# Performance work log

Measured on AMD Instinct MI355X. Metric: run time of the kernel, lower is better.

Reference implementation:

```python
import jax, jax.numpy as jnp
import numpy as np

B, S, H = 2, 1024, 2048
NH, NKV, HD = 16, 8, 128
GROUPS = NH // NKV
THETA = 1000000.0
SPARSITY = 0.4  # q_len > 512 -> vision_sparse_attention_sparsity_ratio
TOP_K = max(1, min(S, int(SPARSITY * S)))


def _rope(q, k, position_ids):
    # inv_freq: [HD/2]
    inv_freq = 1.0 / (THETA ** (jnp.arange(0, HD, 2, dtype=jnp.float32) / HD))
    freqs = position_ids.astype(jnp.float32)[:, :, None] * inv_freq  # [B,S,HD/2]
    emb = jnp.concatenate([freqs, freqs], axis=-1)                   # [B,S,HD]
    cos = jnp.cos(emb)[:, None].astype(q.dtype)  # [B,1,S,HD] (unsqueeze_dim=1)
    sin = jnp.sin(emb)[:, None].astype(q.dtype)
    rot = lambda x: jnp.concatenate([-x[..., HD // 2:], x[..., :HD // 2]], axis=-1)
    return q * cos + rot(q) * sin, k * cos + rot(k) * sin


def setup_inputs() -> dict:
    key = jax.random.key(0)
    ks = jax.random.split(key, 10)
    sc = 0.02
    inp = {
        'hidden_states': jax.random.normal(ks[0], (B, S, H), jnp.float32),
        'wq': jax.random.normal(ks[1], (NH * HD, H), jnp.float32) * sc,
        'bq': jax.random.normal(ks[2], (NH * HD,), jnp.float32) * sc,
        'wk': jax.random.normal(ks[3], (NKV * HD, H), jnp.float32) * sc,
        'bk': jax.random.normal(ks[4], (NKV * HD,), jnp.float32) * sc,
        'wv': jax.random.normal(ks[5], (NKV * HD, H), jnp.float32) * sc,
        'bv': jax.random.normal(ks[6], (NKV * HD,), jnp.float32) * sc,
        'wo': jax.random.normal(ks[7], (H, NH * HD), jnp.float32) * sc,
        'bo': jax.random.normal(ks[8], (H,), jnp.float32) * sc,
        'position_ids': jnp.tile(jnp.arange(S, dtype=jnp.int32)[None, :], (B, 1)),
    }
    return inp


def reference(hidden_states, wq, bq, wk, bk, wv, bv, wo, bo, position_ids):
    # QKV projections -> [B, heads, S, HD]
    q = (hidden_states @ wq.T + bq).reshape(B, S, NH, HD).transpose(0, 2, 1, 3)
    k = (hidden_states @ wk.T + bk).reshape(B, S, NKV, HD).transpose(0, 2, 1, 3)
    v = (hidden_states @ wv.T + bv).reshape(B, S, NKV, HD).transpose(0, 2, 1, 3)

    q, k = _rope(q, k, position_ids)

    # GQA: repeat_interleave KV heads along head axis
    k = jnp.repeat(k, GROUPS, axis=1)
    v = jnp.repeat(v, GROUPS, axis=1)

    scores = jnp.einsum('bhqd,bhkd->bhqk', q, k) / jnp.sqrt(jnp.float32(HD))

    # VectorizedSparseAttention: keep top-k weights per query, -inf elsewhere
    topk_vals = jax.lax.top_k(scores, TOP_K)[0]          # sorted descending
    thresh = topk_vals[..., -1:]                         # k-th largest per row
    sparse = jnp.where(scores >= thresh, scores, -jnp.inf)

    probs = jax.nn.softmax(sparse.astype(jnp.float32), axis=-1).astype(q.dtype)
    attn = jnp.einsum('bhqk,bhkd->bhqd', probs, v)       # [B,NH,S,HD]
    attn = attn.transpose(0, 2, 1, 3).reshape(B, S, NH * HD)
    return attn @ wo.T + bo
```

## Files before the change

### kernel.cpp

```cpp
#include <hip/hip_runtime.h>
#include <hip/hip_bf16.h>

constexpr int B_ = 2, S_ = 1024, H_ = 2048;
constexpr int NH_ = 16, NKV_ = 8, HD_ = 128, GROUPS_ = 2;
constexpr int TOPK_ = 409;
constexpr int QSTRIDE = NH_ * HD_;
constexpr int KSTRIDE = NKV_ * HD_;
constexpr int QB_ = 16;

typedef __attribute__((ext_vector_type(8))) short short8;
typedef __attribute__((ext_vector_type(4))) float f32x4;
typedef __attribute__((ext_vector_type(4))) unsigned u32x4;
typedef __attribute__((ext_vector_type(4))) unsigned short ush4;

__device__ inline unsigned fkey(float x) {
  unsigned u = __float_as_uint(x);
  return (u & 0x80000000u) ? ~u : (u | 0x80000000u);
}
__device__ inline unsigned short bf16_rne(float x) {
  unsigned u = __float_as_uint(x);
  unsigned r = u + 0x7FFFu + ((u >> 16) & 1u);
  return (unsigned short)(r >> 16);
}
__device__ inline float bf16_to_f(unsigned short h) {
  return __uint_as_float((unsigned)h << 16);
}
__device__ inline unsigned packsplit(float x) {
  unsigned u = __float_as_uint(x);
  unsigned r = (u + 0x7FFFu + ((u >> 16) & 1u)) & 0xFFFF0000u;
  float rem = x - __uint_as_float(r);
  unsigned v = __float_as_uint(rem);
  unsigned l = (v + 0x7FFFu + ((v >> 16) & 1u)) >> 16;
  return r | l;
}

#define PERM_HI 0x07060302u
#define PERM_LO 0x05040100u

__device__ inline void unpack8(const unsigned* p, short8& hi, short8& lo) {
  u32x4 w0 = *(const u32x4*)p;
  u32x4 w1 = *(const u32x4*)(p + 4);
  u32x4 h, l;
  h.x = __builtin_amdgcn_perm(w0.y, w0.x, PERM_HI);
  h.y = __builtin_amdgcn_perm(w0.w, w0.z, PERM_HI);
  h.z = __builtin_amdgcn_perm(w1.y, w1.x, PERM_HI);
  h.w = __builtin_amdgcn_perm(w1.w, w1.z, PERM_HI);
  l.x = __builtin_amdgcn_perm(w0.y, w0.x, PERM_LO);
  l.y = __builtin_amdgcn_perm(w0.w, w0.z, PERM_LO);
  l.z = __builtin_amdgcn_perm(w1.y, w1.x, PERM_LO);
  l.w = __builtin_amdgcn_perm(w1.w, w1.z, PERM_LO);
  hi = *(short8*)&h;
  lo = *(short8*)&l;
}
__device__ inline void unpack8r(u32x4 w0, u32x4 w1, short8& hi, short8& lo) {
  u32x4 h, l;
  h.x = __builtin_amdgcn_perm(w0.y, w0.x, PERM_HI);
  h.y = __builtin_amdgcn_perm(w0.w, w0.z, PERM_HI);
  h.z = __builtin_amdgcn_perm(w1.y, w1.x, PERM_HI);
  h.w = __builtin_amdgcn_perm(w1.w, w1.z, PERM_HI);
  l.x = __builtin_amdgcn_perm(w0.y, w0.x, PERM_LO);
  l.y = __builtin_amdgcn_perm(w0.w, w0.z, PERM_LO);
  l.z = __builtin_amdgcn_perm(w1.y, w1.x, PERM_LO);
  l.w = __builtin_amdgcn_perm(w1.w, w1.z, PERM_LO);
  hi = *(short8*)&h;
  lo = *(short8*)&l;
}

template <int TI>
__device__ __forceinline__ void gemm_split_body(
    const float* __restrict__ A, const float* __restrict__ W,
    const float* __restrict__ bias, float* __restrict__ C, int ldc, int c0,
    int K, int m0) {
  __shared__ unsigned short Ah[2][TI * 32 * 32];
  __shared__ unsigned short Al[2][TI * 32 * 32];
  __shared__ unsigned short Wh[2][128 * 32];
  __shared__ unsigned short Wl[2][128 * 32];
  const int tid = threadIdx.x;
  const int lane = tid & 63, wid = tid >> 6;
  const int wrow = (wid >> 1) * (TI * 16), wcol = (wid & 1) * 64;
  const int fm = lane & 15, quad = lane >> 4;
  const int srow = tid >> 3;
  const int skq = (tid & 7) * 4;
  f32x4 acc[TI][4] = {};
  float4 avr[TI], wvr[4];

  auto loadAW = [&](int k0) {
#pragma unroll
    for (int r = 0; r < TI; ++r)
      avr[r] = *(const float4*)&A[(size_t)(m0 + srow + 32 * r) * K + k0 + skq];
#pragma unroll
    for (int r = 0; r < 4; ++r)
      wvr[r] = *(const float4*)&W[(size_t)(srow + 32 * r) * K + k0 + skq];
  };
  auto convWrite = [&](int buf) {
#pragma unroll
    for (int r = 0; r < TI; ++r) {
      const int row = srow + 32 * r;
      const int off =
          row * 32 + ((((skq >> 3) ^ ((row >> 1) & 3)) << 3) | (skq & 7));
      unsigned short h0 = bf16_rne(avr[r].x), h1 = bf16_rne(avr[r].y),
                     h2 = bf16_rne(avr[r].z), h3 = bf16_rne(avr[r].w);
      ush4 hv; hv.x = h0; hv.y = h1; hv.z = h2; hv.w = h3;
      ush4 lv;
      lv.x = bf16_rne(avr[r].x - bf16_to_f(h0));
      lv.y = bf16_rne(avr[r].y - bf16_to_f(h1));
      lv.z = bf16_rne(avr[r].z - bf16_to_f(h2));
      lv.w = bf16_rne(avr[r].w - bf16_to_f(h3));
      *(ush4*)&Ah[buf][off] = hv;
      *(ush4*)&Al[buf][off] = lv;
    }
#pragma unroll
    for (int r = 0; r < 4; ++r) {
      const int row = srow + 32 * r;
      const int off =
          row * 32 + ((((skq >> 3) ^ ((row >> 1) & 3)) << 3) | (skq & 7));
      unsigned short g0 = bf16_rne(wvr[r].x), g1 = bf16_rne(wvr[r].y),
                     g2 = bf16_rne(wvr[r].z), g3 = bf16_rne(wvr[r].w);
      ush4 hv; hv.x = g0; hv.y = g1; hv.z = g2; hv.w = g3;
      ush4 lv;
      lv.x = bf16_rne(wvr[r].x - bf16_to_f(g0));
      lv.y = bf16_rne(wvr[r].y - bf16_to_f(g1));
      lv.z = bf16_rne(wvr[r].z - bf16_to_f(g2));
      lv.w = bf16_rne(wvr[r].w - bf16_to_f(g3));
      *(ush4*)&Wh[buf][off] = hv;
      *(ush4*)&Wl[buf][off] = lv;
    }
  };

  loadAW(0);
  convWrite(0);
  __syncthreads();
  int cur = 0;
  for (int k0 = 0; k0 < K; k0 += 32) {
    const bool more = (k0 + 32) < K;
    if (more) loadAW(k0 + 32);
    short8 ah[TI], al[TI], bh[4], bl[4];
#pragma unroll
    for (int ti = 0; ti < TI; ++ti) {
      const int r = wrow + 16 * ti + fm;
      const int off = r * 32 + ((quad ^ ((r >> 1) & 3)) << 3);
      ah[ti] = *(const short8*)&Ah[cur][off];
      al[ti] = *(const short8*)&Al[cur][off];
    }
#pragma unroll
    for (int tj = 0; tj < 4; ++tj) {
      const int r = wcol + 16 * tj + fm;
      const int off = r * 32 + ((quad ^ ((r >> 1) & 3)) << 3);
      bh[tj] = *(const short8*)&Wh[cur][off];
      bl[tj] = *(const short8*)&Wl[cur][off];
    }
#pragma unroll
    for (int ti = 0; ti < TI; ++ti)
#pragma unroll
      for (int tj = 0; tj < 4; ++tj) {
        acc[ti][tj] = __builtin_amdgcn_mfma_f32_16x16x32_bf16(
            ah[ti], bh[tj], acc[ti][tj], 0, 0, 0);
        acc[ti][tj] = __builtin_amdgcn_mfma_f32_16x16x32_bf16(
            ah[ti], bl[tj], acc[ti][tj], 0, 0, 0);
        acc[ti][tj] = __builtin_amdgcn_mfma_f32_16x16x32_bf16(
            al[ti], bh[tj], acc[ti][tj], 0, 0, 0);
      }
    if (more) convWrite(cur ^ 1);
    __syncthreads();
    cur ^= 1;
  }
#pragma unroll
  for (int tj = 0; tj < 4; ++tj) {
    float bsv = bias[wcol + 16 * tj + fm];
#pragma unroll
    for (int ti = 0; ti < TI; ++ti) {
      int mrow = m0 + wrow + 16 * ti + quad * 4;
      int ncol = c0 + wcol + 16 * tj + fm;
#pragma unroll
      for (int reg = 0; reg < 4; ++reg)
        C[(size_t)(mrow + reg) * ldc + ncol] = acc[ti][tj][reg] + bsv;
    }
  }
}

__global__ __launch_bounds__(256) void gemm_qkv(
    const float* __restrict__ hidden, const float* __restrict__ wq,
    const float* __restrict__ bq, const float* __restrict__ wk,
    const float* __restrict__ bk, const float* __restrict__ wv,
    const float* __restrict__ bv, float* __restrict__ q, float* __restrict__ k,
    float* __restrict__ v) {
  const int n0 = blockIdx.x * 128, m0 = blockIdx.y * 128;
  const float* W;
  const float* bias;
  float* C;
  int ldc, c0;
  if (n0 < QSTRIDE) {
    W = wq + (size_t)n0 * H_; bias = bq + n0; C = q; ldc = QSTRIDE; c0 = n0;
  } else if (n0 < QSTRIDE + KSTRIDE) {
    int nn = n0 - QSTRIDE;
    W = wk + (size_t)nn * H_; bias = bk + nn; C = k; ldc = KSTRIDE; c0 = nn;
  } else {
    int nn = n0 - QSTRIDE - KSTRIDE;
    W = wv + (size_t)nn * H_; bias = bv + nn; C = v; ldc = KSTRIDE; c0 = nn;
  }
  gemm_split_body<4>(hidden, W, bias, C, ldc, c0, H_, m0);
}

template <int TI>
__global__ __launch_bounds__(256) void gemm_split_k(
    const float* __restrict__ A, const float* __restrict__ W,
    const float* __restrict__ bias, float* __restrict__ C, int N, int K) {
  const int n0 = blockIdx.x * 128, m0 = blockIdx.y * (TI * 32);
  gemm_split_body<TI>(A, W + (size_t)n0 * K, bias + n0, C, N, n0, K, m0);
}

__global__ __launch_bounds__(256) void rope_pack(float* __restrict__ qtmp,
                                                 float* __restrict__ ktmp,
                                                 const int* __restrict__ pos_ids) {
  const int s = blockIdx.x, b = blockIdx.y;
  const int t = threadIdx.x;
  __shared__ float fsh[64];
  if (t < 64) fsh[t] = (float)(1.0 / pow(1.0e6, (double)t / 64.0));
  __syncthreads();
  const int pos = pos_ids[b * S_ + s];
#pragma unroll
  for (int it = 0; it < 6; ++it) {
    const int p = t + 256 * it;
    const int slot = p >> 6;
    const int d = p & 63;
    float* base = (slot < NH_)
                      ? qtmp + (size_t)(b * S_ + s) * QSTRIDE + slot * HD_
                      : ktmp + (size_t)(b * S_ + s) * KSTRIDE + (slot - NH_) * HD_;
    float x = base[d], y = base[d + 64];
    unsigned* up = (unsigned*)base;
    float ang = (float)pos * fsh[d];
    float c = cosf(ang), sn = sinf(ang);
    up[d] = packsplit(x * c - y * sn);
    up[d + 64] = packsplit(y * c + x * sn);
  }
}

__global__ __launch_bounds__(256) void vtrans(const float* __restrict__ vtmp,
                                              unsigned* __restrict__ vT) {
  const int s0 = blockIdx.x * 64;
  const int g = blockIdx.y, b = blockIdx.z;
  __shared__ unsigned tile[64][133];
  const int t = threadIdx.x;
  {
    const int row = t >> 5;
    const int c4 = (t & 31) * 4;
    for (int r = 0; r < 64; r += 8) {
      const float* src =
          vtmp + ((size_t)(b * S_ + s0 + row + r) * NKV_ + g) * HD_ + c4;
      float4 xv = *(const float4*)src;
      tile[row + r][c4 + 0] = packsplit(xv.x);
      tile[row + r][c4 + 1] = packsplit(xv.y);
      tile[row + r][c4 + 2] = packsplit(xv.z);
      tile[row + r][c4 + 3] = packsplit(xv.w);
    }
  }
  __syncthreads();
  {
    const int tok4 = (t & 15) * 4;
    const int d0 = t >> 4;
    for (int dd = 0; dd < 128; dd += 16) {
      const int dim = d0 + dd;
      u32x4 o;
      o.x = tile[tok4 + 0][dim];
      o.y = tile[tok4 + 1][dim];
      o.z = tile[tok4 + 2][dim];
      o.w = tile[tok4 + 3][dim];
      *(u32x4*)&vT[(((size_t)(b * NKV_ + g) * HD_ + dim) * S_) + s0 + tok4] = o;
    }
  }
}

constexpr int SCW = 1030;

__global__ __launch_bounds__(512, 4) void attn_kernel(
    unsigned* __restrict__ qpk, const unsigned* __restrict__ kpk,
    const unsigned* __restrict__ vTpk) {
  const int q0 = blockIdx.x * QB_;
  const int h = blockIdx.y, b = blockIdx.z, g = h / GROUPS_;
  const int t = threadIdx.x, lane = t & 63, wid = t >> 6;
  const int fm = lane & 15, quad = lane >> 4;

  __shared__ float sc[QB_ * SCW];
  __shared__ float redmx[8][QB_];
  __shared__ float Zsh[QB_];
  const float scale = 0.08838834764831845f;

  short8 qh[4], ql[4];
  {
    const unsigned* qrow =
        qpk + (size_t)(b * S_ + q0 + fm) * QSTRIDE + h * HD_;
#pragma unroll
    for (int ks = 0; ks < 4; ++ks) {
      u32x4 a0 = *(const u32x4*)&qrow[ks * 32 + quad * 8];
      u32x4 a1 = *(const u32x4*)&qrow[ks * 32 + quad * 8 + 4];
      unpack8r(a0, a1, qh[ks], ql[ks]);
    }
  }

  const unsigned* kg = kpk + (size_t)(b * S_) * KSTRIDE + g * HD_;
  const int krow = wid * 16 + fm;
  const unsigned* kr0 = kg + (size_t)krow * KSTRIDE;
  u32x4 ka[8], kb[8];
#pragma unroll
  for (int ks = 0; ks < 4; ++ks) {
    ka[2 * ks] = *(const u32x4*)&kr0[ks * 32 + quad * 8];
    ka[2 * ks + 1] = *(const u32x4*)&kr0[ks * 32 + quad * 8 + 4];
  }
  f32x4 mxacc = {-1e30f, -1e30f, -1e30f, -1e30f};
#pragma unroll
  for (int tile = 0; tile < 8; ++tile) {
    u32x4* cur = (tile & 1) ? kb : ka;
    u32x4* nxt = (tile & 1) ? ka : kb;
    if (tile < 7) {
      const unsigned* krn = kr0 + (size_t)(tile + 1) * 128 * KSTRIDE;
#pragma unroll
      for (int ks = 0; ks < 4; ++ks) {
        nxt[2 * ks] = *(const u32x4*)&krn[ks * 32 + quad * 8];
        nxt[2 * ks + 1] = *(const u32x4*)&krn[ks * 32 + quad * 8 + 4];
      }
    }
    f32x4 acc = {0.f, 0.f, 0.f, 0.f};
#pragma unroll
    for (int ks = 0; ks < 4; ++ks) {
      short8 bh, bl;
      unpack8r(cur[2 * ks], cur[2 * ks + 1], bh, bl);
      acc = __builtin_amdgcn_mfma_f32_16x16x32_bf16(qh[ks], bh, acc, 0, 0, 0);
      acc = __builtin_amdgcn_mfma_f32_16x16x32_bf16(qh[ks], bl, acc, 0, 0, 0);
      acc = __builtin_amdgcn_mfma_f32_16x16x32_bf16(ql[ks], bh, acc, 0, 0, 0);
    }
    const int key = tile * 128 + krow;
#pragma unroll
    for (int reg = 0; reg < 4; ++reg) {
      float sval = acc[reg] * scale;
      sc[(quad * 4 + reg) * SCW + key] = sval;
      mxacc[reg] = fmaxf(mxacc[reg], sval);
    }
  }
#pragma unroll
  for (int o = 1; o < 16; o <<= 1) {
    mxacc[0] = fmaxf(mxacc[0], __shfl_xor(mxacc[0], o));
    mxacc[1] = fmaxf(mxacc[1], __shfl_xor(mxacc[1], o));
    mxacc[2] = fmaxf(mxacc[2], __shfl_xor(mxacc[2], o));
    mxacc[3] = fmaxf(mxacc[3], __shfl_xor(mxacc[3], o));
  }
  if (fm == 0) {
#pragma unroll
    for (int reg = 0; reg < 4; ++reg) redmx[wid][quad * 4 + reg] = mxacc[reg];
  }
  __syncthreads();

  const int dim = wid * 16 + fm;
  const unsigned* vTr = vTpk + ((size_t)(b * NKV_ + g) * HD_ + dim) * S_;
  u32x4 va[8], vb[8];
#pragma unroll
  for (int ks = 0; ks < 4; ++ks) {
    va[2 * ks] = *(const u32x4*)&vTr[ks * 32 + quad * 8];
    va[2 * ks + 1] = *(const u32x4*)&vTr[ks * 32 + quad * 8 + 4];
  }

  unsigned curA = 0u, curB = 0u;
  {
    unsigned uvA[16], uvB[16];
#pragma unroll
    for (int j = 0; j < 16; ++j)
      uvA[j] = fkey(sc[(2 * wid) * SCW + lane + 64 * j]);
#pragma unroll
    for (int j = 0; j < 16; ++j)
      uvB[j] = fkey(sc[(2 * wid + 1) * SCW + lane + 64 * j]);
    for (int bit = 31; bit >= 0; --bit) {
      const unsigned cA = curA | (1u << bit), cB = curB | (1u << bit);
      int cntA = 0, cntB = 0;
#pragma unroll
      for (int j = 0; j < 16; ++j)
        cntA += __popcll(__ballot(uvA[j] >= cA));
#pragma unroll
      for (int j = 0; j < 16; ++j)
        cntB += __popcll(__ballot(uvB[j] >= cB));
      if (cntA >= TOPK_) curA = cA;
      if (cntB >= TOPK_) curB = cB;
    }
  }
  const unsigned pref = (lane >= 32) ? curB : curA;

  {
    const int qi = t >> 5, li = t & 31;
    const float mx =
        fmaxf(fmaxf(fmaxf(redmx[0][qi], redmx[1][qi]),
                    fmaxf(redmx[2][qi], redmx[3][qi])),
              fmaxf(fmaxf(redmx[4][qi], redmx[5][qi]),
                    fmaxf(redmx[6][qi], redmx[7][qi])));
    unsigned* scp = (unsigned*)&sc[qi * SCW];
    float zloc = 0.f;
#pragma unroll 2
    for (int j = 0; j < 8; ++j) {
      int i4 = li * 4 + 128 * j;
      f32x4 sv = *(const f32x4*)&sc[qi * SCW + i4];
      u32x4 pk;
      float p0 = (fkey(sv.x) >= pref) ? __expf(sv.x - mx) : 0.0f;
      float p1 = (fkey(sv.y) >= pref) ? __expf(sv.y - mx) : 0.0f;
      float p2 = (fkey(sv.z) >= pref) ? __expf(sv.z - mx) : 0.0f;
      float p3 = (fkey(sv.w) >= pref) ? __expf(sv.w - mx) : 0.0f;
      zloc += p0 + p1 + p2 + p3;
      pk.x = packsplit(p0); pk.y = packsplit(p1);
      pk.z = packsplit(p2); pk.w = packsplit(p3);
      *(u32x4*)&scp[i4] = pk;
    }
#pragma unroll
    for (int off = 1; off < 32; off <<= 1) zloc += __shfl_xor(zloc, off);
    if (li == 0) Zsh[qi] = zloc;
  }
  __syncthreads();

  const unsigned* scp2 = (const unsigned*)sc;
  f32x4 oacc = {0.f, 0.f, 0.f, 0.f};
#pragma unroll
  for (int tile = 0; tile < 8; ++tile) {
    u32x4* cur = (tile & 1) ? vb : va;
    u32x4* nxt = (tile & 1) ? va : vb;
    if (tile < 7) {
      const unsigned* vn = vTr + (tile + 1) * 128;
#pragma unroll
      for (int ks = 0; ks < 4; ++ks) {
        nxt[2 * ks] = *(const u32x4*)&vn[ks * 32 + quad * 8];
        nxt[2 * ks + 1] = *(const u32x4*)&vn[ks * 32 + quad * 8 + 4];
      }
    }
#pragma unroll
    for (int ks = 0; ks < 4; ++ks) {
      short8 ph, pl;
      unpack8(&scp2[fm * SCW + tile * 128 + ks * 32 + quad * 8], ph, pl);
      short8 vh, vl;
      unpack8r(cur[2 * ks], cur[2 * ks + 1], vh, vl);
      oacc = __builtin_amdgcn_mfma_f32_16x16x32_bf16(ph, vh, oacc, 0, 0, 0);
      oacc = __builtin_amdgcn_mfma_f32_16x16x32_bf16(ph, vl, oacc, 0, 0, 0);
      oacc = __builtin_amdgcn_mfma_f32_16x16x32_bf16(pl, vh, oacc, 0, 0, 0);
    }
  }

#pragma unroll
  for (int reg = 0; reg < 4; ++reg) {
    const int q = quad * 4 + reg;
    const float invZ = 1.0f / Zsh[q];
    float* outp = (float*)qpk + (size_t)(b * S_ + q0 + q) * QSTRIDE + h * HD_;
    outp[dim] = oacc[reg] * invZ;
  }
}

extern "C" void kernel_launch(void* const* d_in, const int* in_sizes, int n_in,
                              void* d_out, int out_size, void* d_ws,
                              size_t ws_size, hipStream_t stream) {
  const float* hidden = (const float*)d_in[0];
  const float* wq = (const float*)d_in[1];
  const float* bq = (const float*)d_in[2];
  const float* wk = (const float*)d_in[3];
  const float* bk = (const float*)d_in[4];
  const float* wv = (const float*)d_in[5];
  const float* bv = (const float*)d_in[6];
  const float* wo = (const float*)d_in[7];
  const float* bo = (const float*)d_in[8];
  const int* pos = (const int*)d_in[9];
  float* out = (float*)d_out;

  char* ws = (char*)d_ws;
  float* qtmp = (float*)ws;
  float* ktmp = (float*)(ws + ((size_t)16 << 20));
  float* vtmp = (float*)(ws + ((size_t)24 << 20));
  unsigned* vT = (unsigned*)(ws + ((size_t)32 << 20));

  dim3 blk(256);
  gemm_qkv<<<dim3(32, 16), blk, 0, stream>>>(hidden, wq, bq, wk, bk, wv, bv,
                                             qtmp, ktmp, vtmp);
  rope_pack<<<dim3(S_, B_), dim3(256), 0, stream>>>(qtmp, ktmp, pos);
  vtrans<<<dim3(S_ / 64, NKV_, B_), dim3(256), 0, stream>>>(vtmp, vT);
  attn_kernel<<<dim3(S_ / QB_, NH_, B_), dim3(512), 0, stream>>>(
      (unsigned*)qtmp, (const unsigned*)ktmp, vT);
  gemm_split_k<2><<<dim3(H_ / 128, (B_ * S_) / 64), blk, 0, stream>>>(
      qtmp, wo, bo, out, H_, H_);
}
```

Measured before the change: 569.7 us.

## Pre-pack GEMM operands to split bf16, restructure attention loops and top-k count

Adds a pack_inputs kernel that converts hidden states and all weights to packed hi/lo bf16 pairs once per call, so the GEMM inner loops only permute bytes instead of doing float-to-bf16 splitting. The attention kernel writes its output already packed, so the output projection reads packed data. The QK and PV loops are restructured into non-unrolled ping-pong pairs to shrink code size and register pressure. The top-k radix count moves from per-element ballots to per-lane counts reduced with shuffles. The trade-off is an extra full pass over the weights before the GEMMs, plus workspace buffer reuse: vT shares memory with wqP, which is safe only because gemm_qkv finishes before vtrans runs.

```diff
diff --git a/kernel.cpp b/kernel.cpp
--- a/kernel.cpp
+++ b/kernel.cpp
@@ -11,19 +11,11 @@
 typedef __attribute__((ext_vector_type(8))) short short8;
 typedef __attribute__((ext_vector_type(4))) float f32x4;
 typedef __attribute__((ext_vector_type(4))) unsigned u32x4;
-typedef __attribute__((ext_vector_type(4))) unsigned short ush4;
+typedef __attribute__((ext_vector_type(2))) unsigned u32x2;
 
 __device__ inline unsigned fkey(float x) {
   unsigned u = __float_as_uint(x);
   return (u & 0x80000000u) ? ~u : (u | 0x80000000u);
-}
-__device__ inline unsigned short bf16_rne(float x) {
-  unsigned u = __float_as_uint(x);
-  unsigned r = u + 0x7FFFu + ((u >> 16) & 1u);
-  return (unsigned short)(r >> 16);
-}
-__device__ inline float bf16_to_f(unsigned short h) {
-  return __uint_as_float((unsigned)h << 16);
 }
 __device__ inline unsigned packsplit(float x) {
   unsigned u = __float_as_uint(x);
@@ -66,9 +58,33 @@
   lo = *(short8*)&l;
 }
 
+__global__ __launch_bounds__(256) void pack_inputs(
+    const float* __restrict__ hidden, const float* __restrict__ wq,
+    const float* __restrict__ wk, const float* __restrict__ wv,
+    const float* __restrict__ wo, unsigned* __restrict__ hidP,
+    unsigned* __restrict__ wqP, unsigned* __restrict__ wkP,
+    unsigned* __restrict__ wvP, unsigned* __restrict__ woP) {
+  size_t gid = (size_t)blockIdx.x * 256 + threadIdx.x;
+  const float* src;
+  unsigned* dst;
+  size_t off;
+  if (gid < 1048576) { src = hidden; dst = hidP; off = gid; }
+  else if (gid < 2097152) { src = wq; dst = wqP; off = gid - 1048576; }
+  else if (gid < 2621440) { src = wk; dst = wkP; off = gid - 2097152; }
+  else if (gid < 3145728) { src = wv; dst = wvP; off = gid - 2621440; }
+  else { src = wo; dst = woP; off = gid - 3145728; }
+  float4 x = *(const float4*)&src[off * 4];
+  u32x4 p;
+  p.x = packsplit(x.x);
+  p.y = packsplit(x.y);
+  p.z = packsplit(x.z);
+  p.w = packsplit(x.w);
+  *(u32x4*)&dst[off * 4] = p;
+}
+
 template <int TI>
 __device__ __forceinline__ void gemm_split_body(
-    const float* __restrict__ A, const float* __restrict__ W,
+    const unsigned* __restrict__ A, const unsigned* __restrict__ W,
     const float* __restrict__ bias, float* __restrict__ C, int ldc, int c0,
     int K, int m0) {
   __shared__ unsigned short Ah[2][TI * 32 * 32];
@@ -82,15 +98,15 @@
   const int srow = tid >> 3;
   const int skq = (tid & 7) * 4;
   f32x4 acc[TI][4] = {};
-  float4 avr[TI], wvr[4];
+  u32x4 avr[TI], wvr[4];
 
   auto loadAW = [&](int k0) {
 #pragma unroll
     for (int r = 0; r < TI; ++r)
-      avr[r] = *(const float4*)&A[(size_t)(m0 + srow + 32 * r) * K + k0 + skq];
+      avr[r] = *(const u32x4*)&A[(size_t)(m0 + srow + 32 * r) * K + k0 + skq];
 #pragma unroll
     for (int r = 0; r < 4; ++r)
-      wvr[r] = *(const float4*)&W[(size_t)(srow + 32 * r) * K + k0 + skq];
+      wvr[r] = *(const u32x4*)&W[(size_t)(srow + 32 * r) * K + k0 + skq];
   };
   auto convWrite = [&](int buf) {
 #pragma unroll
@@ -98,32 +114,28 @@
       const int row = srow + 32 * r;
       const int off =
           row * 32 + ((((skq >> 3) ^ ((row >> 1) & 3)) << 3) | (skq & 7));
-      unsigned short h0 = bf16_rne(avr[r].x), h1 = bf16_rne(avr[r].y),
-                     h2 = bf16_rne(avr[r].z), h3 = bf16_rne(avr[r].w);
-      ush4 hv; hv.x = h0; hv.y = h1; hv.z = h2; hv.w = h3;
-      ush4 lv;
-      lv.x = bf16_rne(avr[r].x - bf16_to_f(h0));
-      lv.y = bf16_rne(avr[r].y - bf16_to_f(h1));
-      lv.z = bf16_rne(avr[r].z - bf16_to_f(h2));
-      lv.w = bf16_rne(avr[r].w - bf16_to_f(h3));
-      *(ush4*)&Ah[buf][off] = hv;
-      *(ush4*)&Al[buf][off] = lv;
+      u32x4 w = avr[r];
+      u32x2 hi, lo;
+      hi.x = __builtin_amdgcn_perm(w.y, w.x, PERM_HI);
+      hi.y = __builtin_amdgcn_perm(w.w, w.z, PERM_HI);
+      lo.x = __builtin_amdgcn_perm(w.y, w.x, PERM_LO);
+      lo.y = __builtin_amdgcn_perm(w.w, w.z, PERM_LO);
+      *(u32x2*)&Ah[buf][off] = hi;
+      *(u32x2*)&Al[buf][off] = lo;
     }
 #pragma unroll
     for (int r = 0; r < 4; ++r) {
       const int row = srow + 32 * r;
       const int off =
           row * 32 + ((((skq >> 3) ^ ((row >> 1) & 3)) << 3) | (skq & 7));
-      unsigned short g0 = bf16_rne(wvr[r].x), g1 = bf16_rne(wvr[r].y),
-                     g2 = bf16_rne(wvr[r].z), g3 = bf16_rne(wvr[r].w);
-      ush4 hv; hv.x = g0; hv.y = g1; hv.z = g2; hv.w = g3;
-      ush4 lv;
-      lv.x = bf16_rne(wvr[r].x - bf16_to_f(g0));
-      lv.y = bf16_rne(wvr[r].y - bf16_to_f(g1));
-      lv.z = bf16_rne(wvr[r].z - bf16_to_f(g2));
-      lv.w = bf16_rne(wvr[r].w - bf16_to_f(g3));
-      *(ush4*)&Wh[buf][off] = hv;
-      *(ush4*)&Wl[buf][off] = lv;
+      u32x4 w = wvr[r];
+      u32x2 hi, lo;
+      hi.x = __builtin_amdgcn_perm(w.y, w.x, PERM_HI);
+      hi.y = __builtin_amdgcn_perm(w.w, w.z, PERM_HI);
+      lo.x = __builtin_amdgcn_perm(w.y, w.x, PERM_LO);
+      lo.y = __builtin_amdgcn_perm(w.w, w.z, PERM_LO);
+      *(u32x2*)&Wh[buf][off] = hi;
+      *(u32x2*)&Wl[buf][off] = lo;
     }
   };
 
@@ -179,31 +191,29 @@
 }
 
 __global__ __launch_bounds__(256) void gemm_qkv(
-    const float* __restrict__ hidden, const float* __restrict__ wq,
-    const float* __restrict__ bq, const float* __restrict__ wk,
-    const float* __restrict__ bk, const float* __restrict__ wv,
+    const unsigned* __restrict__ hidP, const unsigned* __restrict__ wqP,
+    const float* __restrict__ bq, const unsigned* __restrict__ wkP,
+    const float* __restrict__ bk, const unsigned* __restrict__ wvP,
     const float* __restrict__ bv, float* __restrict__ q, float* __restrict__ k,
     float* __restrict__ v) {
   const int n0 = blockIdx.x * 128, m0 = blockIdx.y * 128;
-  const float* W;
-  const float* bias;
-  float* C;
-  int ldc, c0;
   if (n0 < QSTRIDE) {
-    W = wq + (size_t)n0 * H_; bias = bq + n0; C = q; ldc = QSTRIDE; c0 = n0;
+    gemm_split_body<4>(hidP, wqP + (size_t)n0 * H_, bq + n0, q, QSTRIDE, n0,
+                       H_, m0);
   } else if (n0 < QSTRIDE + KSTRIDE) {
     int nn = n0 - QSTRIDE;
-    W = wk + (size_t)nn * H_; bias = bk + nn; C = k; ldc = KSTRIDE; c0 = nn;
+    gemm_split_body<4>(hidP, wkP + (size_t)nn * H_, bk + nn, k, KSTRIDE, nn,
+                       H_, m0);
   } else {
     int nn = n0 - QSTRIDE - KSTRIDE;
-    W = wv + (size_t)nn * H_; bias = bv + nn; C = v; ldc = KSTRIDE; c0 = nn;
-  }
-  gemm_split_body<4>(hidden, W, bias, C, ldc, c0, H_, m0);
+    gemm_split_body<4>(hidP, wvP + (size_t)nn * H_, bv + nn, v, KSTRIDE, nn,
+                       H_, m0);
+  }
 }
 
 template <int TI>
 __global__ __launch_bounds__(256) void gemm_split_k(
-    const float* __restrict__ A, const float* __restrict__ W,
+    const unsigned* __restrict__ A, const unsigned* __restrict__ W,
     const float* __restrict__ bias, float* __restrict__ C, int N, int K) {
   const int n0 = blockIdx.x * 128, m0 = blockIdx.y * (TI * 32);
   gemm_split_body<TI>(A, W + (size_t)n0 * K, bias + n0, C, N, n0, K, m0);
@@ -301,29 +311,22 @@
   const int krow = wid * 16 + fm;
   const unsigned* kr0 = kg + (size_t)krow * KSTRIDE;
   u32x4 ka[8], kb[8];
-#pragma unroll
-  for (int ks = 0; ks < 4; ++ks) {
-    ka[2 * ks] = *(const u32x4*)&kr0[ks * 32 + quad * 8];
-    ka[2 * ks + 1] = *(const u32x4*)&kr0[ks * 32 + quad * 8 + 4];
-  }
   f32x4 mxacc = {-1e30f, -1e30f, -1e30f, -1e30f};
-#pragma unroll
-  for (int tile = 0; tile < 8; ++tile) {
-    u32x4* cur = (tile & 1) ? kb : ka;
-    u32x4* nxt = (tile & 1) ? ka : kb;
-    if (tile < 7) {
-      const unsigned* krn = kr0 + (size_t)(tile + 1) * 128 * KSTRIDE;
-#pragma unroll
-      for (int ks = 0; ks < 4; ++ks) {
-        nxt[2 * ks] = *(const u32x4*)&krn[ks * 32 + quad * 8];
-        nxt[2 * ks + 1] = *(const u32x4*)&krn[ks * 32 + quad * 8 + 4];
-      }
-    }
+
+  auto k_load = [&](u32x4* kreg, int tile) {
+    const unsigned* kr = kr0 + (size_t)tile * 128 * KSTRIDE;
+#pragma unroll
+    for (int ks = 0; ks < 4; ++ks) {
+      kreg[2 * ks] = *(const u32x4*)&kr[ks * 32 + quad * 8];
+      kreg[2 * ks + 1] = *(const u32x4*)&kr[ks * 32 + quad * 8 + 4];
+    }
+  };
+  auto qk_tile = [&](const u32x4* kreg, int tile) {
     f32x4 acc = {0.f, 0.f, 0.f, 0.f};
 #pragma unroll
     for (int ks = 0; ks < 4; ++ks) {
       short8 bh, bl;
-      unpack8r(cur[2 * ks], cur[2 * ks + 1], bh, bl);
+      unpack8r(kreg[2 * ks], kreg[2 * ks + 1], bh, bl);
       acc = __builtin_amdgcn_mfma_f32_16x16x32_bf16(qh[ks], bh, acc, 0, 0, 0);
       acc = __builtin_amdgcn_mfma_f32_16x16x32_bf16(qh[ks], bl, acc, 0, 0, 0);
       acc = __builtin_amdgcn_mfma_f32_16x16x32_bf16(ql[ks], bh, acc, 0, 0, 0);
@@ -335,7 +338,17 @@
       sc[(quad * 4 + reg) * SCW + key] = sval;
       mxacc[reg] = fmaxf(mxacc[reg], sval);
     }
-  }
+  };
+
+  k_load(ka, 0);
+#pragma unroll 1
+  for (int tp = 0; tp < 4; ++tp) {
+    k_load(kb, 2 * tp + 1);
+    qk_tile(ka, 2 * tp);
+    if (tp < 3) k_load(ka, 2 * tp + 2);
+    qk_tile(kb, 2 * tp + 1);
+  }
+
 #pragma unroll
   for (int o = 1; o < 16; o <<= 1) {
     mxacc[0] = fmaxf(mxacc[0], __shfl_xor(mxacc[0], o));
@@ -352,11 +365,15 @@
   const int dim = wid * 16 + fm;
   const unsigned* vTr = vTpk + ((size_t)(b * NKV_ + g) * HD_ + dim) * S_;
   u32x4 va[8], vb[8];
-#pragma unroll
-  for (int ks = 0; ks < 4; ++ks) {
-    va[2 * ks] = *(const u32x4*)&vTr[ks * 32 + quad * 8];
-    va[2 * ks + 1] = *(const u32x4*)&vTr[ks * 32 + quad * 8 + 4];
-  }
+  auto v_load = [&](u32x4* vreg, int tile) {
+    const unsigned* vr = vTr + tile * 128;
+#pragma unroll
+    for (int ks = 0; ks < 4; ++ks) {
+      vreg[2 * ks] = *(const u32x4*)&vr[ks * 32 + quad * 8];
+      vreg[2 * ks + 1] = *(const u32x4*)&vr[ks * 32 + quad * 8 + 4];
+    }
+  };
+  v_load(va, 0);
 
   unsigned curA = 0u, curB = 0u;
   {
@@ -367,17 +384,19 @@
 #pragma unroll
     for (int j = 0; j < 16; ++j)
       uvB[j] = fkey(sc[(2 * wid + 1) * SCW + lane + 64 * j]);
+#pragma unroll 1
     for (int bit = 31; bit >= 0; --bit) {
       const unsigned cA = curA | (1u << bit), cB = curB | (1u << bit);
-      int cntA = 0, cntB = 0;
-#pragma unroll
-      for (int j = 0; j < 16; ++j)
-        cntA += __popcll(__ballot(uvA[j] >= cA));
-#pragma unroll
-      for (int j = 0; j < 16; ++j)
-        cntB += __popcll(__ballot(uvB[j] >= cB));
-      if (cntA >= TOPK_) curA = cA;
-      if (cntB >= TOPK_) curB = cB;
+      unsigned cntA = 0, cntB = 0;
+#pragma unroll
+      for (int j = 0; j < 16; ++j) cntA += (uvA[j] >= cA) ? 1u : 0u;
+#pragma unroll
+      for (int j = 0; j < 16; ++j) cntB += (uvB[j] >= cB) ? 1u : 0u;
+      unsigned cnt = cntA + (cntB << 16);
+#pragma unroll
+      for (int o = 1; o < 64; o <<= 1) cnt += __shfl_xor(cnt, o);
+      if ((cnt & 0xFFFFu) >= (unsigned)TOPK_) curA = cA;
+      if ((cnt >> 16) >= (unsigned)TOPK_) curB = cB;
     }
   }
   const unsigned pref = (lane >= 32) ? curB : curA;
@@ -413,36 +432,32 @@
 
   const unsigned* scp2 = (const unsigned*)sc;
   f32x4 oacc = {0.f, 0.f, 0.f, 0.f};
-#pragma unroll
-  for (int tile = 0; tile < 8; ++tile) {
-    u32x4* cur = (tile & 1) ? vb : va;
-    u32x4* nxt = (tile & 1) ? va : vb;
-    if (tile < 7) {
-      const unsigned* vn = vTr + (tile + 1) * 128;
-#pragma unroll
-      for (int ks = 0; ks < 4; ++ks) {
-        nxt[2 * ks] = *(const u32x4*)&vn[ks * 32 + quad * 8];
-        nxt[2 * ks + 1] = *(const u32x4*)&vn[ks * 32 + quad * 8 + 4];
-      }
-    }
+  auto pv_tile = [&](const u32x4* vreg, int tile) {
 #pragma unroll
     for (int ks = 0; ks < 4; ++ks) {
       short8 ph, pl;
       unpack8(&scp2[fm * SCW + tile * 128 + ks * 32 + quad * 8], ph, pl);
       short8 vh, vl;
-      unpack8r(cur[2 * ks], cur[2 * ks + 1], vh, vl);
+      unpack8r(vreg[2 * ks], vreg[2 * ks + 1], vh, vl);
       oacc = __builtin_amdgcn_mfma_f32_16x16x32_bf16(ph, vh, oacc, 0, 0, 0);
       oacc = __builtin_amdgcn_mfma_f32_16x16x32_bf16(ph, vl, oacc, 0, 0, 0);
       oacc = __builtin_amdgcn_mfma_f32_16x16x32_bf16(pl, vh, oacc, 0, 0, 0);
     }
+  };
+#pragma unroll 1
+  for (int tp = 0; tp < 4; ++tp) {
+    v_load(vb, 2 * tp + 1);
+    pv_tile(va, 2 * tp);
+    if (tp < 3) v_load(va, 2 * tp + 2);
+    pv_tile(vb, 2 * tp + 1);
   }
 
 #pragma unroll
   for (int reg = 0; reg < 4; ++reg) {
     const int q = quad * 4 + reg;
     const float invZ = 1.0f / Zsh[q];
-    float* outp = (float*)qpk + (size_t)(b * S_ + q0 + q) * QSTRIDE + h * HD_;
-    outp[dim] = oacc[reg] * invZ;
+    unsigned* outp = qpk + (size_t)(b * S_ + q0 + q) * QSTRIDE + h * HD_;
+    outp[dim] = packsplit(oacc[reg] * invZ);
   }
 }
 
@@ -462,18 +477,25 @@
   float* out = (float*)d_out;
 
   char* ws = (char*)d_ws;
-  float* qtmp = (float*)ws;
-  float* ktmp = (float*)(ws + ((size_t)16 << 20));
-  float* vtmp = (float*)(ws + ((size_t)24 << 20));
-  unsigned* vT = (unsigned*)(ws + ((size_t)32 << 20));
+  unsigned* hidP = (unsigned*)(ws);
+  unsigned* wqP = (unsigned*)(ws + ((size_t)16 << 20));
+  unsigned* wkP = (unsigned*)(ws + ((size_t)32 << 20));
+  unsigned* wvP = (unsigned*)(ws + ((size_t)40 << 20));
+  unsigned* woP = (unsigned*)(ws + ((size_t)48 << 20));
+  float* qtmp = (float*)(ws + ((size_t)64 << 20));
+  float* ktmp = (float*)(ws + ((size_t)80 << 20));
+  float* vtmp = (float*)(ws + ((size_t)88 << 20));
+  unsigned* vT = (unsigned*)(ws + ((size_t)16 << 20));
 
   dim3 blk(256);
-  gemm_qkv<<<dim3(32, 16), blk, 0, stream>>>(hidden, wq, bq, wk, bk, wv, bv,
+  pack_inputs<<<dim3(16384), blk, 0, stream>>>(hidden, wq, wk, wv, wo, hidP,
+                                               wqP, wkP, wvP, woP);
+  gemm_qkv<<<dim3(32, 16), blk, 0, stream>>>(hidP, wqP, bq, wkP, bk, wvP, bv,
                                              qtmp, ktmp, vtmp);
-  rope_pack<<<dim3(S_, B_), dim3(256), 0, stream>>>(qtmp, ktmp, pos);
-  vtrans<<<dim3(S_ / 64, NKV_, B_), dim3(256), 0, stream>>>(vtmp, vT);
+  rope_pack<<<dim3(S_, B_), blk, 0, stream>>>(qtmp, ktmp, pos);
+  vtrans<<<dim3(S_ / 64, NKV_, B_), blk, 0, stream>>>(vtmp, vT);
   attn_kernel<<<dim3(S_ / QB_, NH_, B_), dim3(512), 0, stream>>>(
       (unsigned*)qtmp, (const unsigned*)ktmp, vT);
   gemm_split_k<2><<<dim3(H_ / 128, (B_ * S_) / 64), blk, 0, stream>>>(
-      qtmp, wo, bo, out, H_, H_);
-}
+      (const unsigned*)qtmp, woP, bo, out, H_, H_);
+}
```

Result: no change. 579.8 us (+1.8%).
